# Kernel optimization log

Measured on AMD Instinct MI355X. Metric: run time of the kernel, lower is better.

## Reference

```python
import jax, jax.numpy as jnp
import numpy as np

B = 4096      # batch
D_IN = 512    # input_dim
D = 256       # d_model
T = 424       # n_targets
L = 6         # num_layers
EPS = 1e-5    # torch LayerNorm default


def _ln(x, g, b):
    m = jnp.mean(x, axis=-1, keepdims=True)
    v = jnp.var(x, axis=-1, keepdims=True)
    return (x - m) * jax.lax.rsqrt(v + EPS) * g + b


def setup_inputs() -> dict:
    key = jax.random.key(0)
    ks = iter(jax.random.split(key, 32))
    r = lambda shape, s=0.05: jax.random.normal(next(ks), shape, dtype=jnp.float32) * s
    return {
        'x': jax.random.normal(next(ks), (B, D_IN), dtype=jnp.float32),
        'proj_W': r((4, D // 4, D_IN)), 'proj_b': r((4, D // 4)),
        'attn_in_W': r((L, 3 * D, D)), 'attn_in_b': r((L, 3 * D)),
        'attn_out_W': r((L, D, D)), 'attn_out_b': r((L, D)),
        'ln_g': jnp.ones((L, D), jnp.float32), 'ln_b': jnp.zeros((L, D), jnp.float32),
        'ff_W1': r((L, 4 * D, D)), 'ff_b1': r((L, 4 * D)),
        'ff_W2': r((L, D, 4 * D)), 'ff_b2': r((L, D)),
        'cross_in_W': r((3 * D, D)), 'cross_in_b': r((3 * D,)),
        'cross_out_W': r((D, D)), 'cross_out_b': r((D,)),
        'tp_W1': r((T, D // 2, D)), 'tp_b1': r((T, D // 2)),
        'tp_ln_g': jnp.ones((T, D // 2), jnp.float32), 'tp_ln_b': jnp.zeros((T, D // 2), jnp.float32),
        'tp_W2': r((T, D // 4, D // 2)), 'tp_b2': r((T, D // 4)),
        'tp_W3': r((T, D // 4)), 'tp_b3': r((T,)),
    }


def reference(x, proj_W, proj_b, attn_in_W, attn_in_b, attn_out_W, attn_out_b,
              ln_g, ln_b, ff_W1, ff_b1, ff_W2, ff_b2,
              cross_in_W, cross_in_b, cross_out_W, cross_out_b,
              tp_W1, tp_b1, tp_ln_g, tp_ln_b, tp_W2, tp_b2, tp_W3, tp_b3):
    # 4 feature projections -> concat == reshape of stacked einsum  [B, 4, D/4] -> [B, D]
    h = jnp.einsum('bd,pkd->bpk', x, proj_W) + proj_b
    h = h.reshape(h.shape[0], D)

    # 6 transformer blocks on seq_len=1: softmax over a single key == 1, so
    # MHA(x,x,x) reduces exactly to out_proj(v_proj(x)); dropout = identity (eval).
    for i in range(L):
        Wv, bv = attn_in_W[i, 2 * D:], attn_in_b[i, 2 * D:]
        attn = (h @ Wv.T + bv) @ attn_out_W[i].T + attn_out_b[i]
        h = _ln(h + attn, ln_g[i], ln_b[i])          # same norm instance reused
        ff = jax.nn.gelu(h @ ff_W1[i].T + ff_b1[i], approximate=False) @ ff_W2[i].T + ff_b2[i]
        h = _ln(h + ff, ln_g[i], ln_b[i])

    # cross-target attention, also seq_len=1 -> v/out projections only
    Wv, bv = cross_in_W[2 * D:], cross_in_b[2 * D:]
    h = h + ((h @ Wv.T + bv) @ cross_out_W.T + cross_out_b)

    # 424 per-target MLP heads, batched as grouped GEMMs
    t = jnp.einsum('bd,tkd->btk', h, tp_W1) + tp_b1          # [B, T, 128]
    t = jax.nn.relu(_ln(t, tp_ln_g, tp_ln_b))
    t = jax.nn.relu(jnp.einsum('btk,tmk->btm', t, tp_W2) + tp_b2)  # [B, T, 64]
    out = jnp.einsum('btm,tm->bt', t, tp_W3) + tp_b3         # [B, T]
    return out
```

## Files before the change

### kernel.cpp

```cpp
#include <hip/hip_runtime.h>
#include <stdint.h>
#include <utility>
#include <type_traits>

using bf16x8 = __attribute__((ext_vector_type(8))) short;
using f32x4  = __attribute__((ext_vector_type(4))) float;

__device__ __forceinline__ f32x4 mfma16(bf16x8 a, bf16x8 b, f32x4 c) {
  return __builtin_amdgcn_mfma_f32_16x16x32_bf16(a, b, c, 0, 0, 0);
}

__device__ __forceinline__ unsigned short f2b_rne(float f) {
  union { float f; unsigned u; } v; v.f = f;
  unsigned r = v.u + 0x7fffu + ((v.u >> 16) & 1u);
  return (unsigned short)(r >> 16);
}

__device__ __forceinline__ unsigned cvt_pk_bf16(float lo, float hi) {
  unsigned r;
  asm("v_cvt_pk_bf16_f32 %0, %1, %2" : "=v"(r) : "v"(lo), "v"(hi));
  return r;
}

__device__ __forceinline__ void gload16(const void* g, void* l) {
  __builtin_amdgcn_global_load_lds(
      (const __attribute__((address_space(1))) void*)g,
      (__attribute__((address_space(3))) void*)l, 16, 0, 0);
}

template<int N> __device__ __forceinline__ void vmwait() {
  if constexpr (N <= 0)      asm volatile("s_waitcnt vmcnt(0)" ::: "memory");
  else if constexpr (N == 1) asm volatile("s_waitcnt vmcnt(1)" ::: "memory");
  else if constexpr (N == 2) asm volatile("s_waitcnt vmcnt(2)" ::: "memory");
  else if constexpr (N == 3) asm volatile("s_waitcnt vmcnt(3)" ::: "memory");
  else                       asm volatile("s_waitcnt vmcnt(4)" ::: "memory");
}

template<class F, int... Is>
__device__ __forceinline__ void sfor_impl(F&& f, std::integer_sequence<int, Is...>) {
  (f(std::integral_constant<int, Is>{}), ...);
}
template<int N, class F>
__device__ __forceinline__ void sfor(F&& f) {
  sfor_impl(static_cast<F&&>(f), std::make_integer_sequence<int, N>{});
}

__device__ __forceinline__ void stage1(const unsigned short* __restrict__ W, int K,
                                       int col0, int kt, char* slot, int lane) {
  const int ci = lane >> 2, kc = lane & 3;
  const unsigned short* src = W + (size_t)(col0 + ci) * K + kt * 32
                              + (((kc * 16) ^ ((ci & 3) << 4)) >> 1);
  gload16(src, slot);
}

template<int NCG, int AS, int K>
__device__ __forceinline__ void gemm_pipe2(const unsigned short* __restrict__ W, int c0,
                                           const char* __restrict__ abuf,
                                           char* __restrict__ ring, int lane,
                                           f32x4 (&acc)[NCG]) {
  const int r = lane & 15, hi16 = (lane >> 4) << 4;
  const int swz7 = (r & 7) << 4, swz3 = (r & 3) << 4;
  constexpr int NKT = K / 32;
  constexpr int TILES = NCG * NKT;
  stage1(W, K, c0 + (0 % NCG) * 16, 0 / NCG, ring + 0 * 1024, lane);
  if constexpr (TILES > 1) stage1(W, K, c0 + (1 % NCG) * 16, 1 / NCG, ring + 1 * 1024, lane);
  if constexpr (TILES > 2) stage1(W, K, c0 + (2 % NCG) * 16, 2 / NCG, ring + 2 * 1024, lane);
  bf16x8 areg;
  sfor<TILES>([&](auto tc) {
    constexpr int t = tc.value;
    constexpr int kt = t / NCG, cg = t % NCG;
    constexpr int REM = TILES - 1 - t;
    vmwait<(REM < 2 ? REM : 2)>();
    __builtin_amdgcn_sched_barrier(0);
    if constexpr (t + 3 < TILES) {
      constexpr int t3 = t + 3;
      stage1(W, K, c0 + (t3 % NCG) * 16, t3 / NCG, ring + (t3 & 3) * 1024, lane);
    }
    if constexpr (cg == 0)
      areg = *reinterpret_cast<const bf16x8*>(abuf + r * AS + ((kt * 64 + hi16) ^ swz7));
    const bf16x8 b = *reinterpret_cast<const bf16x8*>(
        ring + (t & 3) * 1024 + r * 64 + (hi16 ^ swz3));
    acc[cg] = mfma16(areg, b, acc[cg]);
  });
}

__global__ void f2b_kernel(const float* __restrict__ s, unsigned short* __restrict__ d, int n4) {
  int i = blockIdx.x * 256 + threadIdx.x;
  if (i >= n4) return;
  float4 v = reinterpret_cast<const float4*>(s)[i];
  ushort4 o;
  o.x = f2b_rne(v.x); o.y = f2b_rne(v.y); o.z = f2b_rne(v.z); o.w = f2b_rne(v.w);
  reinterpret_cast<ushort4*>(d)[i] = o;
}

__global__ __launch_bounds__(256) void compose_attn(
    const float* __restrict__ aiW, const float* __restrict__ aib,
    const float* __restrict__ aoW, const float* __restrict__ aob,
    const float* __restrict__ ciW, const float* __restrict__ cib,
    const float* __restrict__ coW, const float* __restrict__ cob,
    unsigned short* __restrict__ wEff, float* __restrict__ bEff) {
  const int mat = blockIdx.y;
  const float* Wo = (mat < 6) ? aoW + (size_t)mat * 65536 : coW;
  const float* Wv = (mat < 6) ? aiW + (size_t)mat * 196608 + 131072 : ciW + 131072;
  const float* bv = (mat < 6) ? aib + mat * 768 + 512 : cib + 512;
  const float* bo = (mat < 6) ? aob + mat * 256 : cob;
  unsigned short* Wd = wEff + (size_t)mat * 65536;
  const int m = blockIdx.x * 16 + (threadIdx.x >> 4);
  const int k0 = (threadIdx.x & 15) * 16;
  float c[16] = {};
  for (int j = 0; j < 256; ++j) {
    const float a = Wo[m * 256 + j];
    const float* Br = Wv + j * 256 + k0;
#pragma unroll
    for (int kk = 0; kk < 16; ++kk) c[kk] = fmaf(a, Br[kk], c[kk]);
  }
#pragma unroll
  for (int kk = 0; kk < 16; ++kk) Wd[m * 256 + k0 + kk] = f2b_rne(c[kk]);
  if (blockIdx.x == 0) {
    const int mm = threadIdx.x;
    float s = 0.f;
    for (int j = 0; j < 256; ++j) s = fmaf(Wo[mm * 256 + j], bv[j], s);
    bEff[mat * 256 + mm] = s + bo[mm];
  }
}

__global__ __launch_bounds__(512, 4) void trunk_fused(
    const unsigned short* __restrict__ xb, const unsigned short* __restrict__ pWb,
    const float* __restrict__ projb,
    const unsigned short* __restrict__ wEff, const float* __restrict__ bEff,
    const unsigned short* __restrict__ f1Wb, const float* __restrict__ f1b,
    const unsigned short* __restrict__ f2Wb, const float* __restrict__ f2bp,
    const float* __restrict__ lng, const float* __restrict__ lnb,
    unsigned short* __restrict__ hbf) {
  __shared__ char hbuf[16 * 512];
  __shared__ char gbuf[16 * 2048];
  __shared__ char ringbuf[8 * 4096];
  __shared__ float red[2][16][8];
  const int tid = threadIdx.x, wid = tid >> 6, lane = tid & 63;
  const int r = lane & 15, hi = lane >> 4;
  const int row0 = blockIdx.x << 4;
  const int colb = wid * 32;
  char* ring = ringbuf + wid * 4096;

#pragma unroll
  for (int i = 0; i < 2; ++i) {
    const int id = tid + i * 512, row = id >> 6, c8 = id & 63;
    bf16x8 v = *reinterpret_cast<const bf16x8*>(xb + (size_t)(row0 + row) * 512 + c8 * 8);
    *reinterpret_cast<bf16x8*>(gbuf + row * 1024 + ((c8 * 16) ^ ((row & 7) << 4))) = v;
  }
  __syncthreads();

  f32x4 hreg[2];

  auto store_hb = [&]() {
#pragma unroll
    for (int cf = 0; cf < 2; ++cf) {
      const int cb = (colb + cf * 16 + r) * 2;
#pragma unroll
      for (int j = 0; j < 4; ++j) {
        const int row = hi * 4 + j;
        *reinterpret_cast<unsigned short*>(hbuf + row * 512 + (cb ^ ((row & 7) << 4))) =
            f2b_rne(hreg[cf][j]);
      }
    }
  };

  auto ln_apply = [&](float gm0, float gm1, float bb0, float bb1) {
    float sum[4], sq[4];
#pragma unroll
    for (int j = 0; j < 4; ++j) {
      const float v0 = hreg[0][j], v1 = hreg[1][j];
      sum[j] = v0 + v1; sq[j] = v0 * v0 + v1 * v1;
    }
#pragma unroll
    for (int m = 1; m < 16; m <<= 1)
#pragma unroll
      for (int j = 0; j < 4; ++j) {
        sum[j] += __shfl_xor(sum[j], m, 64);
        sq[j]  += __shfl_xor(sq[j],  m, 64);
      }
    if (r == 0)
#pragma unroll
      for (int j = 0; j < 4; ++j) {
        red[0][hi * 4 + j][wid] = sum[j];
        red[1][hi * 4 + j][wid] = sq[j];
      }
    __syncthreads();
#pragma unroll
    for (int j = 0; j < 4; ++j) {
      const int row = hi * 4 + j;
      f32x4 p0 = *reinterpret_cast<const f32x4*>(&red[0][row][0]);
      f32x4 p1 = *reinterpret_cast<const f32x4*>(&red[0][row][4]);
      f32x4 q0 = *reinterpret_cast<const f32x4*>(&red[1][row][0]);
      f32x4 q1 = *reinterpret_cast<const f32x4*>(&red[1][row][4]);
      const float ts = p0[0]+p0[1]+p0[2]+p0[3]+p1[0]+p1[1]+p1[2]+p1[3];
      const float tq = q0[0]+q0[1]+q0[2]+q0[3]+q1[0]+q1[1]+q1[2]+q1[3];
      const float mean = ts * (1.f / 256.f);
      const float rstd = rsqrtf(tq * (1.f / 256.f) - mean * mean + 1e-5f);
      hreg[0][j] = (hreg[0][j] - mean) * rstd * gm0 + bb0;
      hreg[1][j] = (hreg[1][j] - mean) * rstd * gm1 + bb1;
    }
  };

  {
    f32x4 acc[2] = {};
    gemm_pipe2<2, 1024, 512>(pWb, colb, gbuf, ring, lane, acc);
    const float bv0 = projb[colb + r], bv1 = projb[colb + 16 + r];
#pragma unroll
    for (int j = 0; j < 4; ++j) { hreg[0][j] = acc[0][j] + bv0; hreg[1][j] = acc[1][j] + bv1; }
  }
  store_hb();
  __syncthreads();

  for (int L = 0; L < 6; ++L) {
    const float gm0 = lng[L * 256 + colb + r],      gm1 = lng[L * 256 + colb + 16 + r];
    const float bb0 = lnb[L * 256 + colb + r],      bb1 = lnb[L * 256 + colb + 16 + r];
    {
      f32x4 acc[2] = {};
      gemm_pipe2<2, 512, 256>(wEff + (size_t)L * 65536, colb, hbuf, ring, lane, acc);
      const float be0 = bEff[L * 256 + colb + r], be1 = bEff[L * 256 + colb + 16 + r];
#pragma unroll
      for (int j = 0; j < 4; ++j) { hreg[0][j] += acc[0][j] + be0; hreg[1][j] += acc[1][j] + be1; }
    }
    ln_apply(gm0, gm1, bb0, bb1);
    store_hb();
    __syncthreads();
    {
      f32x4 accf[8] = {};
      gemm_pipe2<8, 512, 256>(f1Wb + (size_t)L * 262144, wid * 128, hbuf, ring, lane, accf);
#pragma unroll
      for (int cf = 0; cf < 8; ++cf) {
        const int colw = wid * 128 + cf * 16 + r;
        const float bv = f1b[L * 1024 + colw];
        const int cb = colw * 2;
#pragma unroll
        for (int j = 0; j < 4; ++j) {
          float y = accf[cf][j] + bv;
          y = 0.5f * y * (1.f + erff(y * 0.70710678118654752f));
          const int row = hi * 4 + j;
          *reinterpret_cast<unsigned short*>(gbuf + row * 2048 + (cb ^ ((row & 7) << 4))) = f2b_rne(y);
        }
      }
    }
    __syncthreads();
    {
      f32x4 acc[2] = {};
      gemm_pipe2<2, 2048, 1024>(f2Wb + (size_t)L * 262144, colb, gbuf, ring, lane, acc);
      const float be0 = f2bp[L * 256 + colb + r], be1 = f2bp[L * 256 + colb + 16 + r];
#pragma unroll
      for (int j = 0; j < 4; ++j) { hreg[0][j] += acc[0][j] + be0; hreg[1][j] += acc[1][j] + be1; }
    }
    ln_apply(gm0, gm1, bb0, bb1);
    store_hb();
    __syncthreads();
  }

  {
    f32x4 acc[2] = {};
    gemm_pipe2<2, 512, 256>(wEff + 6ull * 65536, colb, hbuf, ring, lane, acc);
    const float be0 = bEff[1536 + colb + r], be1 = bEff[1536 + colb + 16 + r];
#pragma unroll
    for (int j = 0; j < 4; ++j) { hreg[0][j] += acc[0][j] + be0; hreg[1][j] += acc[1][j] + be1; }
  }
#pragma unroll
  for (int cf = 0; cf < 2; ++cf)
#pragma unroll
    for (int j = 0; j < 4; ++j)
      hbf[(size_t)(row0 + hi * 4 + j) * 256 + colb + cf * 16 + r] = f2b_rne(hreg[cf][j]);
}

__global__ __launch_bounds__(512, 2) void phase_d3(
    const unsigned short* __restrict__ hbf, const unsigned short* __restrict__ w1b,
    const float* __restrict__ b1, const float* __restrict__ lng, const float* __restrict__ lnb,
    const unsigned short* __restrict__ w2b, const float* __restrict__ b2,
    const float* __restrict__ w3, const float* __restrict__ b3,
    float* __restrict__ out) {
  __shared__ char sm[149504];
  const int tid = threadIdx.x, wid = tid >> 6, lane = tid & 63;
  const int r = lane & 15, hi = lane >> 4;
  const int sw = (r & 7) << 4;
  const int t = blockIdx.y;

  const unsigned short* w1t = w1b + (size_t)t * 32768;
  const unsigned short* w2t = w2b + (size_t)t * 8192;
#pragma unroll
  for (int i = 0; i < 8; ++i) {
    const int id = tid + i * 512;
    const int c = id >> 5, s = id & 31;
    bf16x8 v = *reinterpret_cast<const bf16x8*>(w1t + c * 256 + s * 8);
    *reinterpret_cast<bf16x8*>(sm + c * 512 + ((s * 16) ^ ((c & 7) << 4))) = v;
  }
#pragma unroll
  for (int i = 0; i < 2; ++i) {
    const int id = tid + i * 512;
    const int c = id >> 4, s = id & 15;
    bf16x8 v = *reinterpret_cast<const bf16x8*>(w2t + c * 128 + s * 8);
    *reinterpret_cast<bf16x8*>(sm + 65536 + c * 256 + ((s * 16) ^ ((c & 7) << 4))) = v;
  }
  {
    float v;
    if (tid < 128)      v = b1 [t * 128 + tid];
    else if (tid < 256) v = lng[t * 128 + tid - 128];
    else if (tid < 384) v = lnb[t * 128 + tid - 256];
    else if (tid < 448) v = b2 [t * 64  + tid - 384];
    else                v = w3 [t * 64  + tid - 448];
    reinterpret_cast<float*>(sm + 81920)[tid] = v;
  }
  __syncthreads();

  const float* cb1 = reinterpret_cast<const float*>(sm + 81920);
  const float* cg  = cb1 + 128;
  const float* cbe = cb1 + 256;
  const float* cb2 = cb1 + 384;
  const float* cw3 = cb1 + 448;
  char* t1w = sm + 83968 + wid * 8192;
  const float b3t = b3[t];
  const int token_b0 = blockIdx.x * 1024;

  for (int tile = 0; tile < 2; ++tile) {
    const int B0 = token_b0 + tile * 512 + wid * 64;

    f32x4 acc1[8][4] = {};
    bf16x8 bc[4], bn[4], b2r[4];
#pragma unroll
    for (int bf = 0; bf < 4; ++bf)
      bc[bf] = *reinterpret_cast<const bf16x8*>(hbf + (size_t)(B0 + bf * 16 + r) * 256 + hi * 8);
#pragma unroll
    for (int bf = 0; bf < 4; ++bf)
      bn[bf] = *reinterpret_cast<const bf16x8*>(hbf + (size_t)(B0 + bf * 16 + r) * 256 + 32 + hi * 8);
#pragma unroll
    for (int ks = 0; ks < 8; ++ks) {
      bf16x8 a[8];
#pragma unroll
      for (int cf = 0; cf < 8; ++cf)
        a[cf] = *reinterpret_cast<const bf16x8*>(sm + (cf * 16 + r) * 512 + ((ks * 64 + hi * 16) ^ sw));
      if (ks < 6) {
#pragma unroll
        for (int bf = 0; bf < 4; ++bf)
          b2r[bf] = *reinterpret_cast<const bf16x8*>(hbf + (size_t)(B0 + bf * 16 + r) * 256 + (ks + 2) * 32 + hi * 8);
      }
      __builtin_amdgcn_s_setprio(1);
#pragma unroll
      for (int cf = 0; cf < 8; ++cf)
#pragma unroll
        for (int bf = 0; bf < 4; ++bf)
          acc1[cf][bf] = mfma16(a[cf], bc[bf], acc1[cf][bf]);
      __builtin_amdgcn_s_setprio(0);
#pragma unroll
      for (int bf = 0; bf < 4; ++bf) { bc[bf] = bn[bf]; bn[bf] = b2r[bf]; }
    }

#pragma unroll
    for (int cf = 0; cf < 8; ++cf) {
      f32x4 b1v = *reinterpret_cast<const f32x4*>(cb1 + cf * 16 + hi * 4);
#pragma unroll
      for (int bf = 0; bf < 4; ++bf) acc1[cf][bf] += b1v;
    }

    float mu[4], rsd[4];
#pragma unroll
    for (int bf = 0; bf < 4; ++bf) {
      float s = 0.f, s2 = 0.f;
#pragma unroll
      for (int cf = 0; cf < 8; ++cf)
#pragma unroll
        for (int j = 0; j < 4; ++j) { float v = acc1[cf][bf][j]; s += v; s2 += v * v; }
      s  += __shfl_xor(s, 16, 64);  s  += __shfl_xor(s, 32, 64);
      s2 += __shfl_xor(s2, 16, 64); s2 += __shfl_xor(s2, 32, 64);
      const float m = s * (1.f / 128.f);
      mu[bf] = m;
      rsd[bf] = rsqrtf(s2 * (1.f / 128.f) - m * m + 1e-5f);
    }

    f32x4 acc2[4][4] = {};
#pragma unroll
    for (int half = 0; half < 2; ++half) {
#pragma unroll
      for (int cf = 0; cf < 8; ++cf) {
        f32x4 gv = *reinterpret_cast<const f32x4*>(cg  + cf * 16 + hi * 4);
        f32x4 bv = *reinterpret_cast<const f32x4*>(cbe + cf * 16 + hi * 4);
#pragma unroll
        for (int bl = 0; bl < 2; ++bl) {
          const int bf = half * 2 + bl;
          float y0 = fmaxf((acc1[cf][bf][0] - mu[bf]) * rsd[bf] * gv[0] + bv[0], 0.f);
          float y1 = fmaxf((acc1[cf][bf][1] - mu[bf]) * rsd[bf] * gv[1] + bv[1], 0.f);
          float y2 = fmaxf((acc1[cf][bf][2] - mu[bf]) * rsd[bf] * gv[2] + bv[2], 0.f);
          float y3 = fmaxf((acc1[cf][bf][3] - mu[bf]) * rsd[bf] * gv[3] + bv[3], 0.f);
          uint2 pk;
          pk.x = cvt_pk_bf16(y0, y1);
          pk.y = cvt_pk_bf16(y2, y3);
          *reinterpret_cast<uint2*>(t1w + (bl * 16 + r) * 256 + ((cf * 32 + hi * 8) ^ sw)) = pk;
        }
      }
#pragma unroll
      for (int ks = 0; ks < 4; ++ks) {
        bf16x8 a2[4];
#pragma unroll
        for (int cf2 = 0; cf2 < 4; ++cf2)
          a2[cf2] = *reinterpret_cast<const bf16x8*>(sm + 65536 + (cf2 * 16 + r) * 256 + ((ks * 64 + hi * 16) ^ sw));
        __builtin_amdgcn_s_setprio(1);
#pragma unroll
        for (int bl = 0; bl < 2; ++bl) {
          bf16x8 bb = *reinterpret_cast<const bf16x8*>(t1w + (bl * 16 + r) * 256 + ((ks * 64 + hi * 16) ^ sw));
#pragma unroll
          for (int cf2 = 0; cf2 < 4; ++cf2)
            acc2[cf2][half * 2 + bl] = mfma16(a2[cf2], bb, acc2[cf2][half * 2 + bl]);
        }
        __builtin_amdgcn_s_setprio(0);
      }
    }

    float s[4] = {0.f, 0.f, 0.f, 0.f};
#pragma unroll
    for (int cf2 = 0; cf2 < 4; ++cf2) {
      f32x4 b2v = *reinterpret_cast<const f32x4*>(cb2 + cf2 * 16 + hi * 4);
      f32x4 w3v = *reinterpret_cast<const f32x4*>(cw3 + cf2 * 16 + hi * 4);
#pragma unroll
      for (int bf = 0; bf < 4; ++bf)
#pragma unroll
        for (int j = 0; j < 4; ++j)
          s[bf] += fmaxf(acc2[cf2][bf][j] + b2v[j], 0.f) * w3v[j];
    }
#pragma unroll
    for (int bf = 0; bf < 4; ++bf) {
      s[bf] += __shfl_xor(s[bf], 16, 64);
      s[bf] += __shfl_xor(s[bf], 32, 64);
      if (hi == 0) out[(size_t)(B0 + bf * 16 + r) * 424 + t] = s[bf] + b3t;
    }
  }
}

extern "C" void kernel_launch(void* const* d_in, const int* in_sizes, int n_in,
                              void* d_out, int out_size, void* d_ws, size_t ws_size,
                              hipStream_t stream) {
  const float* x     = (const float*)d_in[0];
  const float* projW = (const float*)d_in[1];
  const float* projb = (const float*)d_in[2];
  const float* aiW   = (const float*)d_in[3];
  const float* aib   = (const float*)d_in[4];
  const float* aoW   = (const float*)d_in[5];
  const float* aob   = (const float*)d_in[6];
  const float* lng   = (const float*)d_in[7];
  const float* lnbp  = (const float*)d_in[8];
  const float* f1W   = (const float*)d_in[9];
  const float* f1b   = (const float*)d_in[10];
  const float* f2W   = (const float*)d_in[11];
  const float* f2bp  = (const float*)d_in[12];
  const float* ciW   = (const float*)d_in[13];
  const float* cib   = (const float*)d_in[14];
  const float* coW   = (const float*)d_in[15];
  const float* cob   = (const float*)d_in[16];
  const float* tpW1  = (const float*)d_in[17];
  const float* tpb1  = (const float*)d_in[18];
  const float* tplng = (const float*)d_in[19];
  const float* tplnb = (const float*)d_in[20];
  const float* tpW2  = (const float*)d_in[21];
  const float* tpb2  = (const float*)d_in[22];
  const float* tpW3  = (const float*)d_in[23];
  const float* tpb3  = (const float*)d_in[24];
  float* out = (float*)d_out;

  char* ws = (char*)d_ws;
  size_t off = 0;
  auto alloc = [&](size_t n) { char* p = ws + off; off = (off + n + 255) & ~(size_t)255; return p; };
  unsigned short* xb   = (unsigned short*)alloc(4096ull * 512 * 2);
  unsigned short* pWb  = (unsigned short*)alloc(256ull * 512 * 2);
  unsigned short* f1Wb = (unsigned short*)alloc(6ull * 1024 * 256 * 2);
  unsigned short* f2Wb = (unsigned short*)alloc(6ull * 256 * 1024 * 2);
  unsigned short* W1b  = (unsigned short*)alloc(424ull * 128 * 256 * 2);
  unsigned short* W2b  = (unsigned short*)alloc(424ull * 64 * 128 * 2);
  unsigned short* wEff = (unsigned short*)alloc(7ull * 256 * 256 * 2);
  float*          bEff = (float*)alloc(7ull * 256 * 4);
  unsigned short* hbf  = (unsigned short*)alloc(4096ull * 256 * 2);

  auto conv = [&](const float* s, unsigned short* d, size_t n) {
    int n4 = (int)(n >> 2);
    f2b_kernel<<<dim3((n4 + 255) / 256), dim3(256), 0, stream>>>(s, d, n4);
  };
  compose_attn<<<dim3(16, 7), dim3(256), 0, stream>>>(aiW, aib, aoW, aob, ciW, cib, coW, cob, wEff, bEff);
  conv(x, xb, 4096ull * 512);
  conv(projW, pWb, 256ull * 512);
  conv(f1W, f1Wb, 6ull * 1024 * 256);
  conv(f2W, f2Wb, 6ull * 256 * 1024);
  conv(tpW1, W1b, 424ull * 128 * 256);
  conv(tpW2, W2b, 424ull * 64 * 128);

  trunk_fused<<<dim3(256), dim3(512), 0, stream>>>(
      xb, pWb, projb, wEff, bEff, f1Wb, f1b, f2Wb, f2bp, lng, lnbp, hbf);

  phase_d3<<<dim3(4, 424), dim3(512), 0, stream>>>(hbf, W1b, tpb1, tplng, tplnb, W2b, tpb2, tpW3, tpb3, out);
}
```

Before: 570.3 us.

## Widen trunk to 1024 threads with deeper weight pipeline; simplify head prefetch

The trunk kernel now runs 16 waves per block, each owning one 16-column group instead of two, and the weight-staging ring deepens from 4 to 6 slots with 5 tiles in flight. LayerNorm reductions grow to 16 partials per row. Separately, the per-target head kernel drops from a two-ahead to a one-ahead activation prefetch, removes s_setprio hints, and replaces the hardware bf16 pack instruction with software rounding. The wider trunk block is meant to hide more latency per row tile, at the cost of more LDS, more register pressure and more barrier participants. The head-kernel changes look like partial rollbacks and could cost speed.

Result: faster. 537.0 us (-5.8%).

```diff
diff --git a/kernel.cpp b/kernel.cpp
--- a/kernel.cpp
+++ b/kernel.cpp
@@ -14,12 +14,6 @@
   union { float f; unsigned u; } v; v.f = f;
   unsigned r = v.u + 0x7fffu + ((v.u >> 16) & 1u);
   return (unsigned short)(r >> 16);
-}
-
-__device__ __forceinline__ unsigned cvt_pk_bf16(float lo, float hi) {
-  unsigned r;
-  asm("v_cvt_pk_bf16_f32 %0, %1, %2" : "=v"(r) : "v"(lo), "v"(hi));
-  return r;
 }
 
 __device__ __forceinline__ void gload16(const void* g, void* l) {
@@ -33,7 +27,8 @@
   else if constexpr (N == 1) asm volatile("s_waitcnt vmcnt(1)" ::: "memory");
   else if constexpr (N == 2) asm volatile("s_waitcnt vmcnt(2)" ::: "memory");
   else if constexpr (N == 3) asm volatile("s_waitcnt vmcnt(3)" ::: "memory");
-  else                       asm volatile("s_waitcnt vmcnt(4)" ::: "memory");
+  else if constexpr (N == 4) asm volatile("s_waitcnt vmcnt(4)" ::: "memory");
+  else                       asm volatile("s_waitcnt vmcnt(5)" ::: "memory");
 }
 
 template<class F, int... Is>
@@ -54,7 +49,7 @@
 }
 
 template<int NCG, int AS, int K>
-__device__ __forceinline__ void gemm_pipe2(const unsigned short* __restrict__ W, int c0,
+__device__ __forceinline__ void gemm_pipe3(const unsigned short* __restrict__ W, int c0,
                                            const char* __restrict__ abuf,
                                            char* __restrict__ ring, int lane,
                                            f32x4 (&acc)[NCG]) {
@@ -62,24 +57,26 @@
   const int swz7 = (r & 7) << 4, swz3 = (r & 3) << 4;
   constexpr int NKT = K / 32;
   constexpr int TILES = NCG * NKT;
-  stage1(W, K, c0 + (0 % NCG) * 16, 0 / NCG, ring + 0 * 1024, lane);
-  if constexpr (TILES > 1) stage1(W, K, c0 + (1 % NCG) * 16, 1 / NCG, ring + 1 * 1024, lane);
-  if constexpr (TILES > 2) stage1(W, K, c0 + (2 % NCG) * 16, 2 / NCG, ring + 2 * 1024, lane);
+  constexpr int DEPTH = (TILES < 5) ? TILES : 5;
+  sfor<DEPTH>([&](auto pc) {
+    constexpr int p = pc.value;
+    stage1(W, K, c0 + (p % NCG) * 16, p / NCG, ring + (p % 6) * 1024, lane);
+  });
   bf16x8 areg;
   sfor<TILES>([&](auto tc) {
     constexpr int t = tc.value;
     constexpr int kt = t / NCG, cg = t % NCG;
     constexpr int REM = TILES - 1 - t;
-    vmwait<(REM < 2 ? REM : 2)>();
+    vmwait<(REM < 4 ? REM : 4)>();
     __builtin_amdgcn_sched_barrier(0);
-    if constexpr (t + 3 < TILES) {
-      constexpr int t3 = t + 3;
-      stage1(W, K, c0 + (t3 % NCG) * 16, t3 / NCG, ring + (t3 & 3) * 1024, lane);
+    if constexpr (t + 5 < TILES) {
+      constexpr int t5 = t + 5;
+      stage1(W, K, c0 + (t5 % NCG) * 16, t5 / NCG, ring + (t5 % 6) * 1024, lane);
     }
     if constexpr (cg == 0)
       areg = *reinterpret_cast<const bf16x8*>(abuf + r * AS + ((kt * 64 + hi16) ^ swz7));
     const bf16x8 b = *reinterpret_cast<const bf16x8*>(
-        ring + (t & 3) * 1024 + r * 64 + (hi16 ^ swz3));
+        ring + (t % 6) * 1024 + r * 64 + (hi16 ^ swz3));
     acc[cg] = mfma16(areg, b, acc[cg]);
   });
 }
@@ -124,7 +121,7 @@
   }
 }
 
-__global__ __launch_bounds__(512, 4) void trunk_fused(
+__global__ __launch_bounds__(1024) void trunk_fused(
     const unsigned short* __restrict__ xb, const unsigned short* __restrict__ pWb,
     const float* __restrict__ projb,
     const unsigned short* __restrict__ wEff, const float* __restrict__ bEff,
@@ -134,44 +131,37 @@
     unsigned short* __restrict__ hbf) {
   __shared__ char hbuf[16 * 512];
   __shared__ char gbuf[16 * 2048];
-  __shared__ char ringbuf[8 * 4096];
-  __shared__ float red[2][16][8];
+  __shared__ char ringbuf[16 * 6144];
+  __shared__ float red[2][16][16];
   const int tid = threadIdx.x, wid = tid >> 6, lane = tid & 63;
   const int r = lane & 15, hi = lane >> 4;
   const int row0 = blockIdx.x << 4;
-  const int colb = wid * 32;
-  char* ring = ringbuf + wid * 4096;
-
-#pragma unroll
-  for (int i = 0; i < 2; ++i) {
-    const int id = tid + i * 512, row = id >> 6, c8 = id & 63;
+  const int col = wid * 16 + r;
+  char* ring = ringbuf + wid * 6144;
+
+  {
+    const int row = tid >> 6, c8 = tid & 63;
     bf16x8 v = *reinterpret_cast<const bf16x8*>(xb + (size_t)(row0 + row) * 512 + c8 * 8);
     *reinterpret_cast<bf16x8*>(gbuf + row * 1024 + ((c8 * 16) ^ ((row & 7) << 4))) = v;
   }
   __syncthreads();
 
-  f32x4 hreg[2];
+  f32x4 hreg;
 
   auto store_hb = [&]() {
-#pragma unroll
-    for (int cf = 0; cf < 2; ++cf) {
-      const int cb = (colb + cf * 16 + r) * 2;
-#pragma unroll
-      for (int j = 0; j < 4; ++j) {
-        const int row = hi * 4 + j;
-        *reinterpret_cast<unsigned short*>(hbuf + row * 512 + (cb ^ ((row & 7) << 4))) =
-            f2b_rne(hreg[cf][j]);
-      }
+    const int cb = col * 2;
+#pragma unroll
+    for (int j = 0; j < 4; ++j) {
+      const int row = hi * 4 + j;
+      *reinterpret_cast<unsigned short*>(hbuf + row * 512 + (cb ^ ((row & 7) << 4))) =
+          f2b_rne(hreg[j]);
     }
   };
 
-  auto ln_apply = [&](float gm0, float gm1, float bb0, float bb1) {
+  auto ln_apply = [&](float gm, float bb) {
     float sum[4], sq[4];
 #pragma unroll
-    for (int j = 0; j < 4; ++j) {
-      const float v0 = hreg[0][j], v1 = hreg[1][j];
-      sum[j] = v0 + v1; sq[j] = v0 * v0 + v1 * v1;
-    }
+    for (int j = 0; j < 4; ++j) { sum[j] = hreg[j]; sq[j] = hreg[j] * hreg[j]; }
 #pragma unroll
     for (int m = 1; m < 16; m <<= 1)
 #pragma unroll
@@ -189,48 +179,48 @@
 #pragma unroll
     for (int j = 0; j < 4; ++j) {
       const int row = hi * 4 + j;
-      f32x4 p0 = *reinterpret_cast<const f32x4*>(&red[0][row][0]);
-      f32x4 p1 = *reinterpret_cast<const f32x4*>(&red[0][row][4]);
-      f32x4 q0 = *reinterpret_cast<const f32x4*>(&red[1][row][0]);
-      f32x4 q1 = *reinterpret_cast<const f32x4*>(&red[1][row][4]);
-      const float ts = p0[0]+p0[1]+p0[2]+p0[3]+p1[0]+p1[1]+p1[2]+p1[3];
-      const float tq = q0[0]+q0[1]+q0[2]+q0[3]+q1[0]+q1[1]+q1[2]+q1[3];
+      float ts = 0.f, tq = 0.f;
+#pragma unroll
+      for (int q = 0; q < 4; ++q) {
+        f32x4 p = *reinterpret_cast<const f32x4*>(&red[0][row][q * 4]);
+        f32x4 s2 = *reinterpret_cast<const f32x4*>(&red[1][row][q * 4]);
+        ts += p[0] + p[1] + p[2] + p[3];
+        tq += s2[0] + s2[1] + s2[2] + s2[3];
+      }
       const float mean = ts * (1.f / 256.f);
       const float rstd = rsqrtf(tq * (1.f / 256.f) - mean * mean + 1e-5f);
-      hreg[0][j] = (hreg[0][j] - mean) * rstd * gm0 + bb0;
-      hreg[1][j] = (hreg[1][j] - mean) * rstd * gm1 + bb1;
+      hreg[j] = (hreg[j] - mean) * rstd * gm + bb;
     }
   };
 
   {
-    f32x4 acc[2] = {};
-    gemm_pipe2<2, 1024, 512>(pWb, colb, gbuf, ring, lane, acc);
-    const float bv0 = projb[colb + r], bv1 = projb[colb + 16 + r];
-#pragma unroll
-    for (int j = 0; j < 4; ++j) { hreg[0][j] = acc[0][j] + bv0; hreg[1][j] = acc[1][j] + bv1; }
+    f32x4 acc[1] = {};
+    gemm_pipe3<1, 1024, 512>(pWb, wid * 16, gbuf, ring, lane, acc);
+    const float bv = projb[col];
+#pragma unroll
+    for (int j = 0; j < 4; ++j) hreg[j] = acc[0][j] + bv;
   }
   store_hb();
   __syncthreads();
 
   for (int L = 0; L < 6; ++L) {
-    const float gm0 = lng[L * 256 + colb + r],      gm1 = lng[L * 256 + colb + 16 + r];
-    const float bb0 = lnb[L * 256 + colb + r],      bb1 = lnb[L * 256 + colb + 16 + r];
+    const float gm = lng[L * 256 + col], bb = lnb[L * 256 + col];
     {
-      f32x4 acc[2] = {};
-      gemm_pipe2<2, 512, 256>(wEff + (size_t)L * 65536, colb, hbuf, ring, lane, acc);
-      const float be0 = bEff[L * 256 + colb + r], be1 = bEff[L * 256 + colb + 16 + r];
-#pragma unroll
-      for (int j = 0; j < 4; ++j) { hreg[0][j] += acc[0][j] + be0; hreg[1][j] += acc[1][j] + be1; }
-    }
-    ln_apply(gm0, gm1, bb0, bb1);
+      f32x4 acc[1] = {};
+      gemm_pipe3<1, 512, 256>(wEff + (size_t)L * 65536, wid * 16, hbuf, ring, lane, acc);
+      const float be = bEff[L * 256 + col];
+#pragma unroll
+      for (int j = 0; j < 4; ++j) hreg[j] += acc[0][j] + be;
+    }
+    ln_apply(gm, bb);
     store_hb();
     __syncthreads();
     {
-      f32x4 accf[8] = {};
-      gemm_pipe2<8, 512, 256>(f1Wb + (size_t)L * 262144, wid * 128, hbuf, ring, lane, accf);
-#pragma unroll
-      for (int cf = 0; cf < 8; ++cf) {
-        const int colw = wid * 128 + cf * 16 + r;
+      f32x4 accf[4] = {};
+      gemm_pipe3<4, 512, 256>(f1Wb + (size_t)L * 262144, wid * 64, hbuf, ring, lane, accf);
+#pragma unroll
+      for (int cf = 0; cf < 4; ++cf) {
+        const int colw = wid * 64 + cf * 16 + r;
         const float bv = f1b[L * 1024 + colw];
         const int cb = colw * 2;
 #pragma unroll
@@ -244,32 +234,30 @@
     }
     __syncthreads();
     {
-      f32x4 acc[2] = {};
-      gemm_pipe2<2, 2048, 1024>(f2Wb + (size_t)L * 262144, colb, gbuf, ring, lane, acc);
-      const float be0 = f2bp[L * 256 + colb + r], be1 = f2bp[L * 256 + colb + 16 + r];
-#pragma unroll
-      for (int j = 0; j < 4; ++j) { hreg[0][j] += acc[0][j] + be0; hreg[1][j] += acc[1][j] + be1; }
-    }
-    ln_apply(gm0, gm1, bb0, bb1);
+      f32x4 acc[1] = {};
+      gemm_pipe3<1, 2048, 1024>(f2Wb + (size_t)L * 262144, wid * 16, gbuf, ring, lane, acc);
+      const float be = f2bp[L * 256 + col];
+#pragma unroll
+      for (int j = 0; j < 4; ++j) hreg[j] += acc[0][j] + be;
+    }
+    ln_apply(gm, bb);
     store_hb();
     __syncthreads();
   }
 
   {
-    f32x4 acc[2] = {};
-    gemm_pipe2<2, 512, 256>(wEff + 6ull * 65536, colb, hbuf, ring, lane, acc);
-    const float be0 = bEff[1536 + colb + r], be1 = bEff[1536 + colb + 16 + r];
-#pragma unroll
-    for (int j = 0; j < 4; ++j) { hreg[0][j] += acc[0][j] + be0; hreg[1][j] += acc[1][j] + be1; }
-  }
-#pragma unroll
-  for (int cf = 0; cf < 2; ++cf)
-#pragma unroll
-    for (int j = 0; j < 4; ++j)
-      hbf[(size_t)(row0 + hi * 4 + j) * 256 + colb + cf * 16 + r] = f2b_rne(hreg[cf][j]);
-}
-
-__global__ __launch_bounds__(512, 2) void phase_d3(
+    f32x4 acc[1] = {};
+    gemm_pipe3<1, 512, 256>(wEff + 6ull * 65536, wid * 16, hbuf, ring, lane, acc);
+    const float be = bEff[1536 + col];
+#pragma unroll
+    for (int j = 0; j < 4; ++j) hreg[j] += acc[0][j] + be;
+  }
+#pragma unroll
+  for (int j = 0; j < 4; ++j)
+    hbf[(size_t)(row0 + hi * 4 + j) * 256 + col] = f2b_rne(hreg[j]);
+}
+
+__global__ __launch_bounds__(512, 2) void phase_d2(
     const unsigned short* __restrict__ hbf, const unsigned short* __restrict__ w1b,
     const float* __restrict__ b1, const float* __restrict__ lng, const float* __restrict__ lnb,
     const unsigned short* __restrict__ w2b, const float* __restrict__ b2,
@@ -321,33 +309,28 @@
     const int B0 = token_b0 + tile * 512 + wid * 64;
 
     f32x4 acc1[8][4] = {};
-    bf16x8 bc[4], bn[4], b2r[4];
+    bf16x8 bc[4], bn[4];
 #pragma unroll
     for (int bf = 0; bf < 4; ++bf)
       bc[bf] = *reinterpret_cast<const bf16x8*>(hbf + (size_t)(B0 + bf * 16 + r) * 256 + hi * 8);
 #pragma unroll
-    for (int bf = 0; bf < 4; ++bf)
-      bn[bf] = *reinterpret_cast<const bf16x8*>(hbf + (size_t)(B0 + bf * 16 + r) * 256 + 32 + hi * 8);
-#pragma unroll
     for (int ks = 0; ks < 8; ++ks) {
       bf16x8 a[8];
 #pragma unroll
       for (int cf = 0; cf < 8; ++cf)
         a[cf] = *reinterpret_cast<const bf16x8*>(sm + (cf * 16 + r) * 512 + ((ks * 64 + hi * 16) ^ sw));
-      if (ks < 6) {
+      if (ks < 7) {
 #pragma unroll
         for (int bf = 0; bf < 4; ++bf)
-          b2r[bf] = *reinterpret_cast<const bf16x8*>(hbf + (size_t)(B0 + bf * 16 + r) * 256 + (ks + 2) * 32 + hi * 8);
-      }
-      __builtin_amdgcn_s_setprio(1);
+          bn[bf] = *reinterpret_cast<const bf16x8*>(hbf + (size_t)(B0 + bf * 16 + r) * 256 + (ks + 1) * 32 + hi * 8);
+      }
 #pragma unroll
       for (int cf = 0; cf < 8; ++cf)
 #pragma unroll
         for (int bf = 0; bf < 4; ++bf)
           acc1[cf][bf] = mfma16(a[cf], bc[bf], acc1[cf][bf]);
-      __builtin_amdgcn_s_setprio(0);
-#pragma unroll
-      for (int bf = 0; bf < 4; ++bf) { bc[bf] = bn[bf]; bn[bf] = b2r[bf]; }
+#pragma unroll
+      for (int bf = 0; bf < 4; ++bf) bc[bf] = bn[bf];
     }
 
 #pragma unroll
@@ -382,13 +365,16 @@
 #pragma unroll
         for (int bl = 0; bl < 2; ++bl) {
           const int bf = half * 2 + bl;
-          float y0 = fmaxf((acc1[cf][bf][0] - mu[bf]) * rsd[bf] * gv[0] + bv[0], 0.f);
-          float y1 = fmaxf((acc1[cf][bf][1] - mu[bf]) * rsd[bf] * gv[1] + bv[1], 0.f);
-          float y2 = fmaxf((acc1[cf][bf][2] - mu[bf]) * rsd[bf] * gv[2] + bv[2], 0.f);
-          float y3 = fmaxf((acc1[cf][bf][3] - mu[bf]) * rsd[bf] * gv[3] + bv[3], 0.f);
-          uint2 pk;
-          pk.x = cvt_pk_bf16(y0, y1);
-          pk.y = cvt_pk_bf16(y2, y3);
+          unsigned o01, o23;
+          {
+            float y0 = fmaxf((acc1[cf][bf][0] - mu[bf]) * rsd[bf] * gv[0] + bv[0], 0.f);
+            float y1 = fmaxf((acc1[cf][bf][1] - mu[bf]) * rsd[bf] * gv[1] + bv[1], 0.f);
+            float y2 = fmaxf((acc1[cf][bf][2] - mu[bf]) * rsd[bf] * gv[2] + bv[2], 0.f);
+            float y3 = fmaxf((acc1[cf][bf][3] - mu[bf]) * rsd[bf] * gv[3] + bv[3], 0.f);
+            o01 = (unsigned)f2b_rne(y0) | ((unsigned)f2b_rne(y1) << 16);
+            o23 = (unsigned)f2b_rne(y2) | ((unsigned)f2b_rne(y3) << 16);
+          }
+          uint2 pk; pk.x = o01; pk.y = o23;
           *reinterpret_cast<uint2*>(t1w + (bl * 16 + r) * 256 + ((cf * 32 + hi * 8) ^ sw)) = pk;
         }
       }
@@ -398,7 +384,6 @@
 #pragma unroll
         for (int cf2 = 0; cf2 < 4; ++cf2)
           a2[cf2] = *reinterpret_cast<const bf16x8*>(sm + 65536 + (cf2 * 16 + r) * 256 + ((ks * 64 + hi * 16) ^ sw));
-        __builtin_amdgcn_s_setprio(1);
 #pragma unroll
         for (int bl = 0; bl < 2; ++bl) {
           bf16x8 bb = *reinterpret_cast<const bf16x8*>(t1w + (bl * 16 + r) * 256 + ((ks * 64 + hi * 16) ^ sw));
@@ -406,7 +391,6 @@
           for (int cf2 = 0; cf2 < 4; ++cf2)
             acc2[cf2][half * 2 + bl] = mfma16(a2[cf2], bb, acc2[cf2][half * 2 + bl]);
         }
-        __builtin_amdgcn_s_setprio(0);
       }
     }
 
@@ -485,8 +469,8 @@
   conv(tpW1, W1b, 424ull * 128 * 256);
   conv(tpW2, W2b, 424ull * 64 * 128);
 
-  trunk_fused<<<dim3(256), dim3(512), 0, stream>>>(
+  trunk_fused<<<dim3(256), dim3(1024), 0, stream>>>(
       xb, pWb, projb, wEff, bEff, f1Wb, f1b, f2Wb, f2bp, lng, lnbp, hbf);
 
-  phase_d3<<<dim3(4, 424), dim3(512), 0, stream>>>(hbf, W1b, tpb1, tplng, tplnb, W2b, tpb2, tpW3, tpb3, out);
-}
+  phase_d2<<<dim3(4, 424), dim3(512), 0, stream>>>(hbf, W1b, tpb1, tplng, tplnb, W2b, tpb2, tpW3, tpb3, out);
+}
```
